# Performance work log

Measured on AMD Instinct MI355X. Metric: run time of the kernel, lower is better.

## Reference

```python
import jax, jax.numpy as jnp
import numpy as np

WIN = 8
HEADS = 4
KB = 8  # k_bound

# relative position index (static, matches torch meshgrid default 'ij')
_co = np.stack(np.meshgrid(np.arange(WIN), np.arange(WIN), indexing='ij')).reshape(2, -1)
_rel = np.clip(_co[:, :, None] - _co[:, None, :], -(KB - 1), KB - 1).transpose(1, 2, 0).astype(np.int64)
_rel = _rel + (KB - 1)
_rel[:, :, 0] *= 2 * KB - 1
REL_IDX = jnp.asarray(_rel.sum(-1))


def _ln(x, g, b, eps=1e-5):
    m = jnp.mean(x, -1, keepdims=True)
    v = jnp.mean((x - m) ** 2, -1, keepdims=True)
    return (x - m) * jax.lax.rsqrt(v + eps) * g + b


def _conv(x, w, b, pad, groups):
    y = jax.lax.conv_general_dilated(x, w, (1, 1), [(pad, pad), (pad, pad)],
                                     feature_group_count=groups,
                                     dimension_numbers=('NCHW', 'OIHW', 'NCHW'))
    return y + b[None, :, None, None]


def setup_inputs() -> dict:
    key = jax.random.key(0)
    ks = jax.random.split(key, 12)
    B, H, C, HID = 4, 256, 64, 256
    f32 = jnp.float32
    w = lambda k, shape: jax.random.normal(k, shape, f32) * 0.02
    return {
        'x': jax.random.normal(ks[0], (B, H * H, C), f32),
        'norm1_g': jnp.ones((C,), f32), 'norm1_b': jnp.zeros((C,), f32),
        'wq': w(ks[1], (C, C)), 'bq': jnp.zeros((C,), f32),
        'wkv': w(ks[2], (C, 3 * C)), 'bkv': jnp.zeros((3 * C,), f32),
        'rpb': w(ks[3], ((2 * KB - 1) ** 2, HEADS)),
        'pe_dw_w': w(ks[4], (C, 1, 5, 5)), 'pe_dw_b': jnp.zeros((C,), f32),
        'pe_pw_w': w(ks[5], (C, C // HEADS, 1, 1)), 'pe_pw_b': jnp.zeros((C,), f32),
        'proj_w': w(ks[6], (C, C)), 'proj_b': jnp.zeros((C,), f32),
        'norm2_g': jnp.ones((C,), f32), 'norm2_b': jnp.zeros((C,), f32),
        'l1_w': w(ks[7], (C, HID)), 'l1_b': jnp.zeros((HID,), f32),
        'dw_w': w(ks[8], (HID, 1, 3, 3)), 'dw_b': jnp.zeros((HID,), f32),
        'l2_w': w(ks[9], (HID, C)), 'l2_b': jnp.zeros((C,), f32),
    }


def reference(x, norm1_g, norm1_b, wq, bq, wkv, bkv, rpb,
              pe_dw_w, pe_dw_b, pe_pw_w, pe_pw_b, proj_w, proj_b,
              norm2_g, norm2_b, l1_w, l1_b, dw_w, dw_b, l2_w, l2_b):
    B, L, C = x.shape
    H = int(np.sqrt(L))
    hd = C // HEADS
    N = WIN * WIN
    # norm1 + window partition: [B, L, C] -> [B_, N, C]
    h = _ln(x, norm1_g, norm1_b).reshape(B, H // WIN, WIN, H // WIN, WIN, C)
    xw = h.transpose(0, 1, 3, 2, 4, 5).reshape(-1, N, C)
    Bw = xw.shape[0]
    # qkv projection
    q = (xw @ wq + bq).reshape(Bw, N, HEADS, hd).transpose(0, 2, 1, 3)
    kv = (xw @ wkv + bkv).reshape(Bw, N, 3, HEADS, hd).transpose(2, 0, 3, 1, 4)
    k, v, vr = kv[0], kv[1], kv[2]
    # scaled dot-product attn + gathered relative position bias
    attn = jnp.einsum('bhnd,bhmd->bhnm', q * (hd ** -0.5), k)
    bias = rpb[REL_IDX].transpose(2, 0, 1)  # [heads, N, N]
    attn = jax.nn.softmax(attn + bias[None], axis=-1)
    out = jnp.einsum('bhnm,bhmd->bhnd', attn, v).transpose(0, 2, 1, 3).reshape(Bw, N, C)
    vr_img = vr.transpose(0, 1, 3, 2).reshape(Bw, C, WIN, WIN)
    pe = _conv(vr_img, pe_dw_w, pe_dw_b, 2, C)
    pe = _conv(pe, pe_pw_w, pe_pw_b, 0, HEADS)
    pos = pe.reshape(Bw, C, N).transpose(0, 2, 1)
    aw = (out + pos) @ proj_w + proj_b
    # window reverse + residual
    y = aw.reshape(B, H // WIN, H // WIN, WIN, WIN, C).transpose(0, 1, 3, 2, 4, 5).reshape(B, L, C)
    x = x + y
    # LeFF: linear -> gelu -> depthwise 3x3 (+residual) -> linear
    z = jax.nn.gelu(_ln(x, norm2_g, norm2_b) @ l1_w + l1_b, approximate=False)
    HID = z.shape[-1]
    zi = z.reshape(B, H, H, HID).transpose(0, 3, 1, 2)
    zi = jax.nn.gelu(_conv(zi, dw_w, dw_b, 1, HID), approximate=False) + zi
    z = zi.transpose(0, 2, 3, 1).reshape(B, L, HID)
    return x + (z @ l2_w + l2_b)
```

## Files before the change

### kernel.cpp

```cpp
#include <hip/hip_runtime.h>
#include <stdint.h>

#define DEV __device__ __forceinline__

DEV float gelu1(float v) { return 0.5f * v * (1.0f + erff(v * 0.70710678118654752f)); }

DEV float bf2f(uint32_t u16) { union { uint32_t i; float f; } x; x.i = u16 << 16; return x.f; }
DEV uint32_t f2bf(float f) {
    union { float f; uint32_t i; } x; x.f = f;
    return (x.i + 0x7fffu + ((x.i >> 16) & 1u)) >> 16;
}

__global__ __launch_bounds__(256, 2)
void attn_kernel(const float* __restrict__ x,
                 const float* __restrict__ n1g, const float* __restrict__ n1b,
                 const float* __restrict__ wq,  const float* __restrict__ bq,
                 const float* __restrict__ wkv, const float* __restrict__ bkv,
                 const float* __restrict__ rpb,
                 const float* __restrict__ pdww, const float* __restrict__ pdwb,
                 const float* __restrict__ ppww, const float* __restrict__ ppwb,
                 const float* __restrict__ projw, const float* __restrict__ projb,
                 float* __restrict__ xa)
{
    extern __shared__ float sm[];
    float* xn   = sm;
    float* kvb  = sm + 4160;
    float* rpbs = sm + 17216;
    float* outb = xn;
    float* pe1  = kvb;
    float* posb = kvb + 4352;
    float* vrs  = kvb + 8704;

    const int tid = threadIdx.x;
    const int wid = blockIdx.x;
    const int b  = wid >> 10;
    const int wi = (wid >> 5) & 31;
    const int wj = wid & 31;

    if (tid < 225) {
        const float4 v = reinterpret_cast<const float4*>(rpb)[tid];
        rpbs[tid]       = v.x;
        rpbs[232 + tid] = v.y;
        rpbs[464 + tid] = v.z;
        rpbs[696 + tid] = v.w;
    }

    {
        const int t = tid >> 2, q = tid & 3;
        const int grow = wi * 8 + (t >> 3), gcol = wj * 8 + (t & 7);
        const long gbase = ((long)(b * 65536 + grow * 256 + gcol)) * 64;
        const float4* xr = reinterpret_cast<const float4*>(x + gbase);
        float4 v0 = xr[q * 4 + 0], v1 = xr[q * 4 + 1], v2 = xr[q * 4 + 2], v3 = xr[q * 4 + 3];
        float vv[16] = {v0.x, v0.y, v0.z, v0.w, v1.x, v1.y, v1.z, v1.w,
                        v2.x, v2.y, v2.z, v2.w, v3.x, v3.y, v3.z, v3.w};
        float s = 0.f, s2 = 0.f;
#pragma unroll
        for (int i = 0; i < 16; ++i) { s += vv[i]; s2 += vv[i] * vv[i]; }
        s  += __shfl_xor(s, 1);  s  += __shfl_xor(s, 2);
        s2 += __shfl_xor(s2, 1); s2 += __shfl_xor(s2, 2);
        const float m  = s * (1.0f / 64.0f);
        const float rs = rsqrtf(s2 * (1.0f / 64.0f) - m * m + 1e-5f);
        const int c0 = q * 16;
#pragma unroll
        for (int i = 0; i < 16; ++i) {
            const int c = c0 + i;
            xn[t * 65 + c] = (vv[i] - m) * rs * n1g[c] + n1b[c];
        }
    }
    __syncthreads();

    float qrow[16];
    {
        const int p = tid & 63;
        const int hbu = __builtin_amdgcn_readfirstlane((tid >> 6) << 4);
#pragma unroll
        for (int d = 0; d < 16; ++d) qrow[d] = bq[hbu + d];
#pragma unroll 4
        for (int k = 0; k < 64; ++k) {
            const float a = xn[p * 65 + k];
            const float* wr = wq + k * 64 + hbu;
#pragma unroll
            for (int d = 0; d < 16; ++d) qrow[d] = fmaf(a, wr[d], qrow[d]);
        }
#pragma unroll
        for (int d = 0; d < 16; ++d) qrow[d] *= 0.25f;
    }

    {
        const int t = tid & 63;
        const int oc0 = __builtin_amdgcn_readfirstlane((tid >> 6) * 48);
        float acc[48];
#pragma unroll
        for (int i = 0; i < 48; ++i) acc[i] = bkv[oc0 + i];
#pragma unroll 2
        for (int k = 0; k < 64; ++k) {
            const float a = xn[t * 65 + k];
            const float* wr = wkv + k * 192 + oc0;
#pragma unroll
            for (int i = 0; i < 48; ++i) acc[i] = fmaf(a, wr[i], acc[i]);
        }
#pragma unroll
        for (int g = 0; g < 12; ++g) {
            const int c = oc0 + g * 4;
            float* dst = kvb + (c >> 6) * 4352 + t * 68 + (c & 63);
            *reinterpret_cast<float4*>(dst) =
                make_float4(acc[g * 4], acc[g * 4 + 1], acc[g * 4 + 2], acc[g * 4 + 3]);
        }
    }
    __syncthreads();

    {
        const int h = tid >> 6, p = tid & 63;
        const int hb = h << 4;
        const int pbase = ((p >> 3) + 7) * 15 + ((p & 7) + 7);
        const float* rb = rpbs + h * 232;
        float l = 0.f;
        float o[16];
#pragma unroll
        for (int d = 0; d < 16; ++d) o[d] = 0.f;
#pragma unroll 4
        for (int qq = 0; qq < 64; ++qq) {
            const float* kr = kvb + qq * 68 + hb;
            const float4 k0 = *reinterpret_cast<const float4*>(kr);
            const float4 k1 = *reinterpret_cast<const float4*>(kr + 4);
            const float4 k2 = *reinterpret_cast<const float4*>(kr + 8);
            const float4 k3 = *reinterpret_cast<const float4*>(kr + 12);
            float dot = qrow[0]*k0.x + qrow[1]*k0.y + qrow[2]*k0.z + qrow[3]*k0.w
                      + qrow[4]*k1.x + qrow[5]*k1.y + qrow[6]*k1.z + qrow[7]*k1.w
                      + qrow[8]*k2.x + qrow[9]*k2.y + qrow[10]*k2.z + qrow[11]*k2.w
                      + qrow[12]*k3.x + qrow[13]*k3.y + qrow[14]*k3.z + qrow[15]*k3.w;
            const int ridx = pbase - ((qq >> 3) * 15 + (qq & 7));
            const float e = __expf(dot + rb[ridx] - 8.0f);
            l += e;
            const float* vr = kvb + 4352 + qq * 68 + hb;
            const float4 v0 = *reinterpret_cast<const float4*>(vr);
            const float4 v1 = *reinterpret_cast<const float4*>(vr + 4);
            const float4 v2 = *reinterpret_cast<const float4*>(vr + 8);
            const float4 v3 = *reinterpret_cast<const float4*>(vr + 12);
            o[0]  += e * v0.x; o[1]  += e * v0.y; o[2]  += e * v0.z; o[3]  += e * v0.w;
            o[4]  += e * v1.x; o[5]  += e * v1.y; o[6]  += e * v1.z; o[7]  += e * v1.w;
            o[8]  += e * v2.x; o[9]  += e * v2.y; o[10] += e * v2.z; o[11] += e * v2.w;
            o[12] += e * v3.x; o[13] += e * v3.y; o[14] += e * v3.z; o[15] += e * v3.w;
        }
        const float inv = 1.0f / l;
#pragma unroll
        for (int d = 0; d < 16; ++d) outb[p * 65 + hb + d] = o[d] * inv;
    }
    __syncthreads();

    {
        const int ch = tid & 63, pg = tid >> 6;
        float wdw[25];
#pragma unroll
        for (int u = 0; u < 25; ++u) wdw[u] = pdww[ch * 25 + u];
        const float bd = pdwb[ch];
#pragma unroll
        for (int ii = 0; ii < 16; ++ii) {
            const int pp = pg * 16 + ii;
            const int py = pp >> 3, px = pp & 7;
            float s = bd;
#pragma unroll
            for (int dy = -2; dy <= 2; ++dy) {
                const int yy = py + dy; if (yy < 0 || yy > 7) continue;
#pragma unroll
                for (int dx = -2; dx <= 2; ++dx) {
                    const int xx = px + dx; if (xx < 0 || xx > 7) continue;
                    s += vrs[(yy * 8 + xx) * 68 + ch] * wdw[(dy + 2) * 5 + (dx + 2)];
                }
            }
            pe1[pp * 65 + ch] = s;
        }
        const int g = ch >> 4;
        float wp[16];
#pragma unroll
        for (int jj = 0; jj < 16; ++jj) wp[jj] = ppww[ch * 16 + jj];
        const float bp = ppwb[ch];
#pragma unroll
        for (int ii = 0; ii < 16; ++ii) {
            const int pp = pg * 16 + ii;
            const float* pr = pe1 + pp * 65 + g * 16;
            float s = bp;
#pragma unroll
            for (int jj = 0; jj < 16; ++jj) s += pr[jj] * wp[jj];
            posb[pp * 65 + ch] = s;
        }
    }
    __syncthreads();

    {
        const int t = tid & 63;
        const int oc0 = __builtin_amdgcn_readfirstlane((tid >> 6) << 4);
        float acc[16];
#pragma unroll
        for (int i = 0; i < 16; ++i) acc[i] = projb[oc0 + i];
#pragma unroll 2
        for (int k = 0; k < 64; ++k) {
            const float a = outb[t * 65 + k] + posb[t * 65 + k];
            const float* wr = projw + k * 64 + oc0;
#pragma unroll
            for (int i = 0; i < 16; ++i) acc[i] = fmaf(a, wr[i], acc[i]);
        }
        const int grow = wi * 8 + (t >> 3), gcol = wj * 8 + (t & 7);
        const long gi = ((long)(b * 65536 + grow * 256 + gcol)) * 64 + oc0;
#pragma unroll
        for (int g = 0; g < 4; ++g) {
            const float4 xr = *reinterpret_cast<const float4*>(x + gi + 4 * g);
            float4 r;
            r.x = xr.x + acc[4 * g + 0]; r.y = xr.y + acc[4 * g + 1];
            r.z = xr.z + acc[4 * g + 2]; r.w = xr.w + acc[4 * g + 3];
            *reinterpret_cast<float4*>(xa + gi + 4 * g) = r;
        }
    }
}

__global__ __launch_bounds__(512, 4)
void leff1_kernel(const float* __restrict__ xa,
                  const float* __restrict__ n2g, const float* __restrict__ n2b,
                  const float* __restrict__ l1w, const float* __restrict__ l1b,
                  uint16_t* __restrict__ zout)
{
    extern __shared__ float sm[];
    float* xn = sm;
    const int tid = threadIdx.x;
    const long t0 = (long)blockIdx.x * 64;

    {
        const int t = tid >> 3, q = tid & 7;
        const float4* xr = reinterpret_cast<const float4*>(xa + (t0 + t) * 64);
        const float4 v0 = xr[q * 2], v1 = xr[q * 2 + 1];
        float vv[8] = {v0.x, v0.y, v0.z, v0.w, v1.x, v1.y, v1.z, v1.w};
        float s = 0.f, s2 = 0.f;
#pragma unroll
        for (int i = 0; i < 8; ++i) { s += vv[i]; s2 += vv[i] * vv[i]; }
        s  += __shfl_xor(s, 1);  s  += __shfl_xor(s, 2);  s  += __shfl_xor(s, 4);
        s2 += __shfl_xor(s2, 1); s2 += __shfl_xor(s2, 2); s2 += __shfl_xor(s2, 4);
        const float m  = s * (1.0f / 64.0f);
        const float rs = rsqrtf(s2 * (1.0f / 64.0f) - m * m + 1e-5f);
        const int c0 = q * 8;
#pragma unroll
        for (int i = 0; i < 8; ++i) {
            const int c = c0 + i;
            xn[t * 65 + c] = (vv[i] - m) * rs * n2g[c] + n2b[c];
        }
    }
    __syncthreads();

    {
        const int tok = tid & 63;
        const int oc0 = __builtin_amdgcn_readfirstlane((tid >> 6) * 32);
        float acc[32];
#pragma unroll
        for (int i = 0; i < 32; ++i) acc[i] = l1b[oc0 + i];
#pragma unroll 2
        for (int k = 0; k < 64; ++k) {
            const float a = xn[tok * 65 + k];
            const float* wr = l1w + k * 256 + oc0;
#pragma unroll
            for (int i = 0; i < 32; ++i) acc[i] = fmaf(a, wr[i], acc[i]);
        }
        uint16_t* zb = zout + (t0 + tok) * 256 + oc0;
#pragma unroll
        for (int g = 0; g < 4; ++g) {
            uint4 pk;
            pk.x = f2bf(gelu1(acc[g*8+0])) | (f2bf(gelu1(acc[g*8+1])) << 16);
            pk.y = f2bf(gelu1(acc[g*8+2])) | (f2bf(gelu1(acc[g*8+3])) << 16);
            pk.z = f2bf(gelu1(acc[g*8+4])) | (f2bf(gelu1(acc[g*8+5])) << 16);
            pk.w = f2bf(gelu1(acc[g*8+6])) | (f2bf(gelu1(acc[g*8+7])) << 16);
            *reinterpret_cast<uint4*>(zb + g * 8) = pk;
        }
    }
}

__global__ __launch_bounds__(256, 2)
void leff2_kernel(const uint16_t* __restrict__ zin,
                  const float* __restrict__ dww, const float* __restrict__ dwb,
                  const float* __restrict__ l2w, const float* __restrict__ l2b,
                  const float* xa,
                  float* out)
{
    extern __shared__ float sm[];
    float* zh = sm;
    const int tid = threadIdx.x;
    const int bb = blockIdx.x >> 10;
    const int ty = (blockIdx.x >> 5) & 31, tx = blockIdx.x & 31;
    const int py0 = ty * 8, px0 = tx * 8;

    const int pix = tid & 63;
    const int ocb = __builtin_amdgcn_readfirstlane((tid >> 6) << 4);
    float4 acc[4];
#pragma unroll
    for (int j = 0; j < 4; ++j)
        acc[j] = *reinterpret_cast<const float4*>(l2b + ocb + 4 * j);

    for (int H = 0; H < 2; ++H) {
        {
            const int c32 = tid & 31, pr = tid >> 5;
#pragma unroll
            for (int it = 0; it < 13; ++it) {
                const int pp = it * 8 + pr;
                if (pp < 100) {
                    const int hy = pp / 10, hx = pp % 10;
                    const int gy = py0 + hy - 1, gx = px0 + hx - 1;
                    float4 v = make_float4(0.f, 0.f, 0.f, 0.f);
                    if (gy >= 0 && gy < 256 && gx >= 0 && gx < 256) {
                        const long gi = ((long)(bb * 65536 + gy * 256 + gx)) * 256
                                        + H * 128 + c32 * 4;
                        const uint2 d = *reinterpret_cast<const uint2*>(zin + gi);
                        v.x = bf2f(d.x & 0xffffu); v.y = bf2f(d.x >> 16);
                        v.z = bf2f(d.y & 0xffffu); v.w = bf2f(d.y >> 16);
                    }
                    *reinterpret_cast<float4*>(&zh[pp * 132 + c32 * 4]) = v;
                }
            }
        }
        __syncthreads();

        float4 zc[8];
        {
            const int c32 = tid & 31, pg = tid >> 5;
            const int ch0 = H * 128 + c32 * 4;
            float4 wd[9];
#pragma unroll
            for (int u = 0; u < 9; ++u)
                wd[u] = make_float4(dww[(ch0 + 0) * 9 + u], dww[(ch0 + 1) * 9 + u],
                                    dww[(ch0 + 2) * 9 + u], dww[(ch0 + 3) * 9 + u]);
            const float4 bd = *reinterpret_cast<const float4*>(dwb + ch0);
#pragma unroll
            for (int ii = 0; ii < 8; ++ii) {
                const int pp = pg * 8 + ii;
                const int hy = (pp >> 3) + 1, hx = (pp & 7) + 1;
                float4 s = bd;
                float4 zi = make_float4(0.f, 0.f, 0.f, 0.f);
#pragma unroll
                for (int dy = -1; dy <= 1; ++dy)
#pragma unroll
                    for (int dx = -1; dx <= 1; ++dx) {
                        const float4 t = *reinterpret_cast<const float4*>(
                            &zh[((hy + dy) * 10 + hx + dx) * 132 + c32 * 4]);
                        if (dy == 0 && dx == 0) zi = t;
                        const float4 w = wd[(dy + 1) * 3 + (dx + 1)];
                        s.x += t.x * w.x; s.y += t.y * w.y;
                        s.z += t.z * w.z; s.w += t.w * w.w;
                    }
                zc[ii] = make_float4(gelu1(s.x) + zi.x, gelu1(s.y) + zi.y,
                                     gelu1(s.z) + zi.z, gelu1(s.w) + zi.w);
            }
        }
        __syncthreads();
        {
            const int c32 = tid & 31, pg = tid >> 5;
#pragma unroll
            for (int ii = 0; ii < 8; ++ii) {
                const int pp = pg * 8 + ii;
                const int hy = (pp >> 3) + 1, hx = (pp & 7) + 1;
                *reinterpret_cast<float4*>(&zh[(hy * 10 + hx) * 132 + c32 * 4]) = zc[ii];
            }
        }
        __syncthreads();

        {
            const int hy = (pix >> 3) + 1, hx = (pix & 7) + 1;
            const float* zrow = &zh[(hy * 10 + hx) * 132];
#pragma unroll 4
            for (int k4 = 0; k4 < 32; ++k4) {
                const float4 a4 = *reinterpret_cast<const float4*>(zrow + k4 * 4);
                const float av[4] = {a4.x, a4.y, a4.z, a4.w};
#pragma unroll
                for (int kk = 0; kk < 4; ++kk) {
                    const int kg = H * 128 + k4 * 4 + kk;
                    const float* wr = l2w + kg * 64 + ocb;
#pragma unroll
                    for (int j = 0; j < 4; ++j) {
                        const float4 w = *reinterpret_cast<const float4*>(wr + 4 * j);
                        acc[j].x += av[kk] * w.x; acc[j].y += av[kk] * w.y;
                        acc[j].z += av[kk] * w.z; acc[j].w += av[kk] * w.w;
                    }
                }
            }
        }
        __syncthreads();
    }

    {
        const long gi = ((long)(bb * 65536 + (py0 + (pix >> 3)) * 256 + px0 + (pix & 7))) * 64 + ocb;
#pragma unroll
        for (int j = 0; j < 4; ++j) {
            const float4 xr = *reinterpret_cast<const float4*>(xa + gi + 4 * j);
            float4 r;
            r.x = acc[j].x + xr.x; r.y = acc[j].y + xr.y;
            r.z = acc[j].z + xr.z; r.w = acc[j].w + xr.w;
            *reinterpret_cast<float4*>(out + gi + 4 * j) = r;
        }
    }
}

extern "C" void kernel_launch(void* const* d_in, const int* in_sizes, int n_in,
                              void* d_out, int out_size, void* d_ws, size_t ws_size,
                              hipStream_t stream) {
    (void)in_sizes; (void)n_in; (void)out_size; (void)ws_size;
    const float* x    = (const float*)d_in[0];
    const float* n1g  = (const float*)d_in[1];
    const float* n1b  = (const float*)d_in[2];
    const float* wq   = (const float*)d_in[3];
    const float* bq   = (const float*)d_in[4];
    const float* wkv  = (const float*)d_in[5];
    const float* bkv  = (const float*)d_in[6];
    const float* rpb  = (const float*)d_in[7];
    const float* pdww = (const float*)d_in[8];
    const float* pdwb = (const float*)d_in[9];
    const float* ppww = (const float*)d_in[10];
    const float* ppwb = (const float*)d_in[11];
    const float* prw  = (const float*)d_in[12];
    const float* prb  = (const float*)d_in[13];
    const float* n2g  = (const float*)d_in[14];
    const float* n2b  = (const float*)d_in[15];
    const float* l1w  = (const float*)d_in[16];
    const float* l1b  = (const float*)d_in[17];
    const float* dww  = (const float*)d_in[18];
    const float* dwb  = (const float*)d_in[19];
    const float* l2w  = (const float*)d_in[20];
    const float* l2b  = (const float*)d_in[21];
    float* out = (float*)d_out;

    float* xa = out;
    uint16_t* zp = (uint16_t*)d_ws;

    const int ATTN_LDS  = 18144 * 4;
    const int LEFF1_LDS = 4160 * 4;
    const int LEFF2_LDS = 13200 * 4;

    (void)hipFuncSetAttribute((const void*)attn_kernel,
                              hipFuncAttributeMaxDynamicSharedMemorySize, ATTN_LDS);

    attn_kernel<<<4096, dim3(256), ATTN_LDS, stream>>>(
        x, n1g, n1b, wq, bq, wkv, bkv, rpb, pdww, pdwb, ppww, ppwb, prw, prb, xa);
    leff1_kernel<<<4096, dim3(512), LEFF1_LDS, stream>>>(xa, n2g, n2b, l1w, l1b, zp);
    leff2_kernel<<<4096, dim3(256), LEFF2_LDS, stream>>>(zp, dww, dwb, l2w, l2b, xa, out);
}
```

Before: 871.2 us.

## Use fp16 MFMA for LeFF first linear with swizzled LDS tiles

Replaces the scalar FMA loop of the LeFF first linear layer with 16x16x32 fp16 MFMA instructions. Normalized activations and weights are staged in XOR-swizzled LDS, and an optional pre-pass converts l1_w to a packed fp16 layout in workspace. The intermediate z is now stored as fp16 instead of bf16, and the output is staged through LDS for coalesced stores. This trades precision of the activations and weights for matrix-core throughput and adds a small prep kernel launch on every call.

```diff
diff --git a/kernel.cpp b/kernel.cpp
--- a/kernel.cpp
+++ b/kernel.cpp
@@ -5,11 +5,11 @@
 
 DEV float gelu1(float v) { return 0.5f * v * (1.0f + erff(v * 0.70710678118654752f)); }
 
-DEV float bf2f(uint32_t u16) { union { uint32_t i; float f; } x; x.i = u16 << 16; return x.f; }
-DEV uint32_t f2bf(float f) {
-    union { float f; uint32_t i; } x; x.f = f;
-    return (x.i + 0x7fffu + ((x.i >> 16) & 1u)) >> 16;
-}
+using half8 = __attribute__((ext_vector_type(8))) _Float16;
+using f32x4 = __attribute__((ext_vector_type(4))) float;
+
+DEV float h2f_lo(uint32_t u) { union { uint16_t s; _Float16 h; } c; c.s = (uint16_t)(u & 0xffffu); return (float)c.h; }
+DEV float h2f_hi(uint32_t u) { union { uint16_t s; _Float16 h; } c; c.s = (uint16_t)(u >> 16); return (float)c.h; }
 
 __global__ __launch_bounds__(256, 2)
 void attn_kernel(const float* __restrict__ x,
@@ -213,60 +213,128 @@
     }
 }
 
-__global__ __launch_bounds__(512, 4)
+__global__ void prep_w1(const float* __restrict__ l1w, uint16_t* __restrict__ w1p)
+{
+    const int oc = threadIdx.x;
+    for (int k = 0; k < 64; ++k) {
+        union { _Float16 h; uint16_t u; } cv;
+        cv.h = (_Float16)l1w[k * 256 + oc];
+        const int kb = k >> 3;
+        w1p[oc * 64 + (((kb ^ (oc & 7)) << 3) | (k & 7))] = cv.u;
+    }
+}
+
+template<bool PREPPED>
+__global__ __launch_bounds__(256, 4)
 void leff1_kernel(const float* __restrict__ xa,
                   const float* __restrict__ n2g, const float* __restrict__ n2b,
-                  const float* __restrict__ l1w, const float* __restrict__ l1b,
+                  const uint16_t* __restrict__ w1p, const float* __restrict__ l1w,
+                  const float* __restrict__ l1b,
                   uint16_t* __restrict__ zout)
 {
-    extern __shared__ float sm[];
-    float* xn = sm;
+    __shared__ uint16_t smh[20480];
+    _Float16* xnh = (_Float16*)smh;
+    _Float16* w1h = (_Float16*)(smh + 4096);
+    _Float16* osg = (_Float16*)smh;
+
     const int tid = threadIdx.x;
     const long t0 = (long)blockIdx.x * 64;
 
     {
-        const int t = tid >> 3, q = tid & 7;
+        const int t = tid >> 2, q = tid & 3;
         const float4* xr = reinterpret_cast<const float4*>(xa + (t0 + t) * 64);
-        const float4 v0 = xr[q * 2], v1 = xr[q * 2 + 1];
-        float vv[8] = {v0.x, v0.y, v0.z, v0.w, v1.x, v1.y, v1.z, v1.w};
+        float4 v0 = xr[q * 4 + 0], v1 = xr[q * 4 + 1], v2 = xr[q * 4 + 2], v3 = xr[q * 4 + 3];
+        float vv[16] = {v0.x, v0.y, v0.z, v0.w, v1.x, v1.y, v1.z, v1.w,
+                        v2.x, v2.y, v2.z, v2.w, v3.x, v3.y, v3.z, v3.w};
         float s = 0.f, s2 = 0.f;
 #pragma unroll
-        for (int i = 0; i < 8; ++i) { s += vv[i]; s2 += vv[i] * vv[i]; }
-        s  += __shfl_xor(s, 1);  s  += __shfl_xor(s, 2);  s  += __shfl_xor(s, 4);
-        s2 += __shfl_xor(s2, 1); s2 += __shfl_xor(s2, 2); s2 += __shfl_xor(s2, 4);
+        for (int i = 0; i < 16; ++i) { s += vv[i]; s2 += vv[i] * vv[i]; }
+        s  += __shfl_xor(s, 1);  s  += __shfl_xor(s, 2);
+        s2 += __shfl_xor(s2, 1); s2 += __shfl_xor(s2, 2);
         const float m  = s * (1.0f / 64.0f);
         const float rs = rsqrtf(s2 * (1.0f / 64.0f) - m * m + 1e-5f);
-        const int c0 = q * 8;
+        const int c0 = q * 16;
+        half8 h0, h1;
 #pragma unroll
         for (int i = 0; i < 8; ++i) {
-            const int c = c0 + i;
-            xn[t * 65 + c] = (vv[i] - m) * rs * n2g[c] + n2b[c];
-        }
-    }
-    __syncthreads();
-
-    {
-        const int tok = tid & 63;
-        const int oc0 = __builtin_amdgcn_readfirstlane((tid >> 6) * 32);
-        float acc[32];
-#pragma unroll
-        for (int i = 0; i < 32; ++i) acc[i] = l1b[oc0 + i];
-#pragma unroll 2
-        for (int k = 0; k < 64; ++k) {
-            const float a = xn[tok * 65 + k];
-            const float* wr = l1w + k * 256 + oc0;
-#pragma unroll
-            for (int i = 0; i < 32; ++i) acc[i] = fmaf(a, wr[i], acc[i]);
-        }
-        uint16_t* zb = zout + (t0 + tok) * 256 + oc0;
-#pragma unroll
-        for (int g = 0; g < 4; ++g) {
-            uint4 pk;
-            pk.x = f2bf(gelu1(acc[g*8+0])) | (f2bf(gelu1(acc[g*8+1])) << 16);
-            pk.y = f2bf(gelu1(acc[g*8+2])) | (f2bf(gelu1(acc[g*8+3])) << 16);
-            pk.z = f2bf(gelu1(acc[g*8+4])) | (f2bf(gelu1(acc[g*8+5])) << 16);
-            pk.w = f2bf(gelu1(acc[g*8+6])) | (f2bf(gelu1(acc[g*8+7])) << 16);
-            *reinterpret_cast<uint4*>(zb + g * 8) = pk;
+            h0[i] = (_Float16)((vv[i]     - m) * rs * n2g[c0 + i]     + n2b[c0 + i]);
+            h1[i] = (_Float16)((vv[8 + i] - m) * rs * n2g[c0 + 8 + i] + n2b[c0 + 8 + i]);
+        }
+        const int kb0 = q * 2;
+        *reinterpret_cast<half8*>(&xnh[t * 64 + (((kb0    ) ^ (t & 7)) << 3)]) = h0;
+        *reinterpret_cast<half8*>(&xnh[t * 64 + (((kb0 + 1) ^ (t & 7)) << 3)]) = h1;
+    }
+    if (PREPPED) {
+        const uint4* src = reinterpret_cast<const uint4*>(w1p);
+        uint4* dst = reinterpret_cast<uint4*>(w1h);
+#pragma unroll
+        for (int i = 0; i < 8; ++i) dst[tid + i * 256] = src[tid + i * 256];
+    } else {
+        const int oc = tid;
+#pragma unroll
+        for (int kb = 0; kb < 8; ++kb) {
+            half8 h;
+#pragma unroll
+            for (int j = 0; j < 8; ++j)
+                h[j] = (_Float16)l1w[(kb * 8 + j) * 256 + oc];
+            *reinterpret_cast<half8*>(&w1h[oc * 64 + (((kb ^ (oc & 7)) << 3))]) = h;
+        }
+    }
+    __syncthreads();
+
+    const int w    = tid >> 6;
+    const int lane = tid & 63;
+    const int l15  = lane & 15, l4 = lane >> 4;
+    f32x4 acc[4][4];
+#pragma unroll
+    for (int ot = 0; ot < 4; ++ot) {
+        const float bb = l1b[w * 64 + ot * 16 + l15];
+#pragma unroll
+        for (int tt = 0; tt < 4; ++tt) { acc[tt][ot][0] = bb; acc[tt][ot][1] = bb; acc[tt][ot][2] = bb; acc[tt][ot][3] = bb; }
+    }
+#pragma unroll
+    for (int kk = 0; kk < 2; ++kk) {
+        half8 af[4];
+#pragma unroll
+        for (int tt = 0; tt < 4; ++tt) {
+            const int row = tt * 16 + l15;
+            af[tt] = *reinterpret_cast<const half8*>(
+                &xnh[row * 64 + (((kk * 4 + l4) ^ (row & 7)) << 3)]);
+        }
+#pragma unroll
+        for (int ot = 0; ot < 4; ++ot) {
+            const int oc = w * 64 + ot * 16 + l15;
+            const half8 bf = *reinterpret_cast<const half8*>(
+                &w1h[oc * 64 + (((kk * 4 + l4) ^ (oc & 7)) << 3)]);
+#pragma unroll
+            for (int tt = 0; tt < 4; ++tt)
+                acc[tt][ot] = __builtin_amdgcn_mfma_f32_16x16x32_f16(af[tt], bf, acc[tt][ot], 0, 0, 0);
+        }
+    }
+    __syncthreads();
+
+    {
+        _Float16* myo = osg + w * (64 * 72);
+#pragma unroll
+        for (int tt = 0; tt < 4; ++tt)
+#pragma unroll
+            for (int ot = 0; ot < 4; ++ot)
+#pragma unroll
+                for (int r = 0; r < 4; ++r) {
+                    const int tok = tt * 16 + l4 * 4 + r;
+                    myo[tok * 72 + ot * 16 + l15] = (_Float16)gelu1(acc[tt][ot][r]);
+                }
+    }
+    __syncthreads();
+    {
+        _Float16* myo = osg + w * (64 * 72);
+        uint16_t* zb = zout + t0 * 256 + w * 64;
+#pragma unroll
+        for (int i = 0; i < 8; ++i) {
+            const int c  = lane + i * 64;
+            const int tok = c >> 3, p8 = c & 7;
+            const uint4 v = *reinterpret_cast<const uint4*>(&myo[tok * 72 + p8 * 8]);
+            *reinterpret_cast<uint4*>(zb + (long)tok * 256 + p8 * 8) = v;
         }
     }
 }
@@ -306,8 +374,8 @@
                         const long gi = ((long)(bb * 65536 + gy * 256 + gx)) * 256
                                         + H * 128 + c32 * 4;
                         const uint2 d = *reinterpret_cast<const uint2*>(zin + gi);
-                        v.x = bf2f(d.x & 0xffffu); v.y = bf2f(d.x >> 16);
-                        v.z = bf2f(d.y & 0xffffu); v.w = bf2f(d.y >> 16);
+                        v.x = h2f_lo(d.x); v.y = h2f_hi(d.x);
+                        v.z = h2f_lo(d.y); v.w = h2f_hi(d.y);
                     }
                     *reinterpret_cast<float4*>(&zh[pp * 132 + c32 * 4]) = v;
                 }
@@ -397,7 +465,7 @@
 extern "C" void kernel_launch(void* const* d_in, const int* in_sizes, int n_in,
                               void* d_out, int out_size, void* d_ws, size_t ws_size,
                               hipStream_t stream) {
-    (void)in_sizes; (void)n_in; (void)out_size; (void)ws_size;
+    (void)in_sizes; (void)n_in; (void)out_size;
     const float* x    = (const float*)d_in[0];
     const float* n1g  = (const float*)d_in[1];
     const float* n1b  = (const float*)d_in[2];
@@ -423,10 +491,11 @@
     float* out = (float*)d_out;
 
     float* xa = out;
-    uint16_t* zp = (uint16_t*)d_ws;
+    uint16_t* zp  = (uint16_t*)d_ws;
+    uint16_t* w1p = (uint16_t*)((char*)d_ws + 134217728ull);
+    const bool prepped = ws_size >= 134217728ull + 32768ull;
 
     const int ATTN_LDS  = 18144 * 4;
-    const int LEFF1_LDS = 4160 * 4;
     const int LEFF2_LDS = 13200 * 4;
 
     (void)hipFuncSetAttribute((const void*)attn_kernel,
@@ -434,6 +503,11 @@
 
     attn_kernel<<<4096, dim3(256), ATTN_LDS, stream>>>(
         x, n1g, n1b, wq, bq, wkv, bkv, rpb, pdww, pdwb, ppww, ppwb, prw, prb, xa);
-    leff1_kernel<<<4096, dim3(512), LEFF1_LDS, stream>>>(xa, n2g, n2b, l1w, l1b, zp);
+    if (prepped) {
+        prep_w1<<<1, dim3(256), 0, stream>>>(l1w, w1p);
+        leff1_kernel<true><<<4096, dim3(256), 0, stream>>>(xa, n2g, n2b, w1p, l1w, l1b, zp);
+    } else {
+        leff1_kernel<false><<<4096, dim3(256), 0, stream>>>(xa, n2g, n2b, w1p, l1w, l1b, zp);
+    }
     leff2_kernel<<<4096, dim3(256), LEFF2_LDS, stream>>>(zp, dww, dwb, l2w, l2b, xa, out);
 }
```

Result: faster. 812.2 us (-6.8%).
